# Kernel optimization log

Hardware: AMD Instinct MI355X
Metric: run time of the kernel (lower is better)

Reference implementation:

```python
import jax, jax.numpy as jnp
import numpy as np

D_MODEL = 1024
POOL = 2048
K = 16
D_FF = 4096
N_HEADS = 16
TEMP = 1.0
EPS = 1e-5


def _ln(x, g, b):
    mu = jnp.mean(x, axis=-1, keepdims=True)
    var = jnp.mean((x - mu) ** 2, axis=-1, keepdims=True)
    return (x - mu) * jax.lax.rsqrt(var + EPS) * g + b


def setup_inputs() -> dict:
    key = jax.random.key(0)
    ks = jax.random.split(key, 12)
    s = 0.02
    return {
        "x": jax.random.normal(ks[0], (4, 1024, D_MODEL), jnp.float32),
        "w_router": s * jax.random.normal(ks[1], (D_MODEL, POOL), jnp.float32),
        "b_router": jnp.zeros((POOL,), jnp.float32),
        "firing": s * jax.random.normal(ks[2], (POOL, D_FF), jnp.float32),
        "w_pool_out": s * jax.random.normal(ks[3], (D_FF, D_MODEL), jnp.float32),
        "b_pool_out": jnp.zeros((D_MODEL,), jnp.float32),
        "w_in": s * jax.random.normal(ks[4], (D_MODEL, 3 * D_MODEL), jnp.float32),
        "b_in": jnp.zeros((3 * D_MODEL,), jnp.float32),
        "w_attn_out": s * jax.random.normal(ks[5], (D_MODEL, D_MODEL), jnp.float32),
        "b_attn_out": jnp.zeros((D_MODEL,), jnp.float32),
        "g1": jnp.ones((D_MODEL,), jnp.float32),
        "beta1": jnp.zeros((D_MODEL,), jnp.float32),
        "g2": jnp.ones((D_MODEL,), jnp.float32),
        "beta2": jnp.zeros((D_MODEL,), jnp.float32),
    }


def reference(x, w_router, b_router, firing, w_pool_out, b_pool_out,
              w_in, b_in, w_attn_out, b_attn_out, g1, beta1, g2, beta2):
    B, S, D = x.shape
    Hd = D // N_HEADS
    # --- Context router: score every neuron, select top-k, softmax weights ---
    scores = x @ w_router + b_router                      # [B,S,P]
    top_vals, top_idx = jax.lax.top_k(scores, K)          # [B,S,K]
    weights = jax.nn.softmax(top_vals / TEMP, axis=-1)    # [B,S,K]
    # --- Neuron pool: gather firing patterns, weighted combine, GELU, project ---
    patterns = firing[top_idx]                            # [B,S,K,d_ff] gather
    combined = jnp.einsum('bsk,bskf->bsf', weights, patterns)  # [B,S,d_ff]
    neuron_out = jax.nn.gelu(combined, approximate=False) @ w_pool_out + b_pool_out  # [B,S,D]
    # --- Self-attention over neuron_out (dropout inactive at eval) ---
    qkv = neuron_out @ w_in + b_in                        # [B,S,3D]
    q, k, v = jnp.split(qkv, 3, axis=-1)
    q = q.reshape(B, S, N_HEADS, Hd).transpose(0, 2, 1, 3)
    k = k.reshape(B, S, N_HEADS, Hd).transpose(0, 2, 1, 3)
    v = v.reshape(B, S, N_HEADS, Hd).transpose(0, 2, 1, 3)
    logits = jnp.einsum('bhqd,bhkd->bhqk', q, k) / jnp.sqrt(jnp.float32(Hd))
    probs = jax.nn.softmax(logits, axis=-1)
    ctx = jnp.einsum('bhqk,bhkd->bhqd', probs, v)
    ctx = ctx.transpose(0, 2, 1, 3).reshape(B, S, D)
    attn_out = ctx @ w_attn_out + b_attn_out
    # --- Residuals + norms ---
    h = _ln(x + attn_out, g1, beta1)
    out = _ln(h + neuron_out, g2, beta2)
    return out
```

## Files before the change

kernel.cpp:

```cpp
#include <hip/hip_runtime.h>
#include <math.h>

typedef __attribute__((ext_vector_type(8))) __bf16 bf16x8;
typedef __attribute__((ext_vector_type(4))) __bf16 bf16x4;
typedef __attribute__((ext_vector_type(4))) float f32x4;

#define DEV static __device__ __forceinline__

DEV float b2f(unsigned short u){ union{unsigned i; float f;} c; c.i=((unsigned)u)<<16; return c.f; }
DEV unsigned short f2b(float f){
  union{float f; unsigned u;} c; c.f=f;
  unsigned r = 0x7FFFu + ((c.u>>16)&1u);
  return (unsigned short)((c.u + r)>>16);
}
DEV unsigned pack2(float a, float b){ return (unsigned)f2b(a) | ((unsigned)f2b(b)<<16); }
DEV float gelu_exact(float x){ return 0.5f*x*(1.f+erff(x*0.70710678118654752f)); }

typedef __attribute__((address_space(1))) void gas_void;
typedef __attribute__((address_space(3))) void las_void;
DEV void gload_lds16(const unsigned short* g, unsigned short* l){
  __builtin_amdgcn_global_load_lds((const gas_void*)g, (las_void*)l, 16, 0, 0);
}

template<int N> DEV void waitcnt_vm(){
  if constexpr(N==0)      asm volatile("s_waitcnt vmcnt(0)" ::: "memory");
  else if constexpr(N==2) asm volatile("s_waitcnt vmcnt(2)" ::: "memory");
  else if constexpr(N==3) asm volatile("s_waitcnt vmcnt(3)" ::: "memory");
  else if constexpr(N==4) asm volatile("s_waitcnt vmcnt(4)" ::: "memory");
  else if constexpr(N==6) asm volatile("s_waitcnt vmcnt(6)" ::: "memory");
  else if constexpr(N==8) asm volatile("s_waitcnt vmcnt(8)" ::: "memory");
  else                    asm volatile("s_waitcnt vmcnt(0)" ::: "memory");
}

__global__ __launch_bounds__(256) void k_cast_bf16(const float* __restrict__ in,
                                                   unsigned short* __restrict__ out, long n4)
{
  long i = (long)blockIdx.x*256 + threadIdx.x;
  if (i >= n4) return;
  float4 v = ((const float4*)in)[i];
  ushort4 o; o.x=f2b(v.x); o.y=f2b(v.y); o.z=f2b(v.z); o.w=f2b(v.w);
  ((ushort4*)out)[i] = o;
}

__global__ __launch_bounds__(256) void k_transpose_cast(const float* __restrict__ in,
                                                        unsigned short* __restrict__ out,
                                                        int R, int C)
{
  __shared__ float tile[32][33];
  const int tc = blockIdx.x*32, tr = blockIdx.y*32;
  {
    const int r = threadIdx.x>>3, c4 = (threadIdx.x&7)*4;
    float4 v = *(const float4*)&in[(long)(tr+r)*C + tc+c4];
    tile[r][c4+0]=v.x; tile[r][c4+1]=v.y; tile[r][c4+2]=v.z; tile[r][c4+3]=v.w;
  }
  __syncthreads();
  {
    const int c = threadIdx.x>>3, r4 = (threadIdx.x&7)*4;
    ushort4 o;
    o.x = f2b(tile[r4+0][c]); o.y = f2b(tile[r4+1][c]);
    o.z = f2b(tile[r4+2][c]); o.w = f2b(tile[r4+3][c]);
    *(ushort4*)&out[(long)(tc+c)*R + tr+r4] = o;
  }
}

template<int WR, int WC, int FM, int FN, int OMODE>
__global__ __launch_bounds__(WR*WC*64, 2) void k_gemm_bt(
  const unsigned short* __restrict__ A, long lda, long sAb,
  const unsigned short* __restrict__ Bt, long ldb, long sBb,
  float* __restrict__ Cf, unsigned short* __restrict__ Cb, long ldc, long sCb,
  const float* __restrict__ bias, int Kiters)
{
  constexpr int WAVES = WR*WC;
  constexpr int BM = WR*FM*16, BN = WC*FN*16;
  constexpr int AR16 = BM/16, TOT16 = (BM+BN)/16;
  constexpr int UNITS = TOT16/WAVES;
  static_assert(TOT16 % WAVES == 0, "stage units must split across waves");
  __shared__ __align__(16) unsigned short S[3][TOT16*512];
  const int tid = threadIdx.x;
  const int wave = tid>>6, lane = tid&63;
  const int wr = wave/WC, wc = wave%WC;
  const int l15 = lane&15, lhi = lane>>4;
  const int lrow = lane>>2;
  const int lcol = ((lane&3) ^ ((lrow>>1)&3))*8;

  const int gx = gridDim.x;
  const int nwg = gx*gridDim.y;
  const int id = blockIdx.y*gx + blockIdx.x;
  const int sid = (id&7)*(nwg>>3) + (id>>3);
  const long bm = (long)(sid / gx)*BM, bn = (long)(sid % gx)*BN;

  const unsigned short* Ab  = A  + (long)blockIdx.z*sAb + bm*lda;
  const unsigned short* Btb = Bt + (long)blockIdx.z*sBb + bn*ldb;

  f32x4 acc[FM][FN];
  #pragma unroll
  for (int i=0;i<FM;i++)
    #pragma unroll
    for (int j=0;j<FN;j++) acc[i][j] = (f32x4){0.f,0.f,0.f,0.f};

  auto STAGE = [&](int kt, int buf){
    const long k0 = (long)kt*32;
    #pragma unroll
    for (int u=0; u<UNITS; ++u) {
      const int t = wave + u*WAVES;
      const unsigned short* g;
      if (t < AR16) g = Ab  + (long)(t*16 + lrow)*lda + k0 + lcol;
      else          g = Btb + (long)((t-AR16)*16 + lrow)*ldb + k0 + lcol;
      gload_lds16(g, &S[buf][t*512]);
    }
  };
  auto COMPUTE = [&](int buf){
    const unsigned short* Sb = S[buf];
    bf16x8 bfr[FN];
    #pragma unroll
    for (int j=0;j<FN;j++) {
      const int r = wc*(FN*16) + j*16 + l15;
      bfr[j] = *(const bf16x8*)&Sb[BM*32 + r*32 + ((lhi ^ ((r>>1)&3))*8)];
    }
    #pragma unroll
    for (int i=0;i<FM;i++) {
      const int r = wr*(FM*16) + i*16 + l15;
      bf16x8 a = *(const bf16x8*)&Sb[r*32 + ((lhi ^ ((r>>1)&3))*8)];
      #pragma unroll
      for (int j=0;j<FN;j++)
        acc[i][j] = __builtin_amdgcn_mfma_f32_16x16x32_bf16(a, bfr[j], acc[i][j], 0,0,0);
    }
  };

  STAGE(0, 0);
  if (Kiters > 1) STAGE(1, 1);
  for (int kt=0; kt<Kiters; ++kt) {
    if (kt+1 < Kiters) waitcnt_vm<UNITS>();
    else               waitcnt_vm<0>();
    __builtin_amdgcn_s_barrier();
    __builtin_amdgcn_sched_barrier(0);
    COMPUTE(kt%3);
    if (kt+2 < Kiters) STAGE(kt+2, (kt+2)%3);
  }

  #pragma unroll
  for (int i=0;i<FM;i++) {
    #pragma unroll
    for (int j=0;j<FN;j++) {
      long col = bn + wc*(FN*16) + j*16 + l15;
      float bb = bias ? bias[col] : 0.f;
      #pragma unroll
      for (int q=0;q<4;q++) {
        long row = bm + wr*(FM*16) + i*16 + lhi*4 + q;
        float v = acc[i][j][q] + bb;
        long off = (long)blockIdx.z*sCb + row*ldc + col;
        if constexpr (OMODE==0 || OMODE==2) Cf[off] = v;
        if constexpr (OMODE==1 || OMODE==2) Cb[off] = f2b(v);
      }
    }
  }
}

__global__ __launch_bounds__(256) void k_combine_bias_bf16(
    const float* __restrict__ p, long sz, const float* __restrict__ bias,
    unsigned short* __restrict__ outb)
{
  const long t = blockIdx.x;
  const int tid = threadIdx.x;
  float4 a = ((const float4*)(p + t*1024))[tid];
  float4 b = ((const float4*)(p + sz + t*1024))[tid];
  float4 bi = ((const float4*)bias)[tid];
  ushort4 o;
  o.x = f2b(a.x+b.x+bi.x); o.y = f2b(a.y+b.y+bi.y);
  o.z = f2b(a.z+b.z+bi.z); o.w = f2b(a.w+b.w+bi.w);
  ((ushort4*)(outb + t*1024))[tid] = o;
}

__global__ __launch_bounds__(256) void k_topk_softmax(const float* __restrict__ scores,
                                                      int* __restrict__ topidx,
                                                      float* __restrict__ topw)
{
  const int tid = threadIdx.x, wave = tid>>6, lane = tid&63;
  const long t = blockIdx.x;
  const float* row = scores + t*2048;
  const int base = wave*512 + lane*8;
  unsigned k0,k1,k2,k3,k4,k5,k6,k7;
  {
    float4 a = *(const float4*)(row + base);
    float4 b = *(const float4*)(row + base + 4);
    float v[8] = {a.x,a.y,a.z,a.w,b.x,b.y,b.z,b.w};
    unsigned kk[8];
    #pragma unroll
    for (int e=0;e<8;e++){
      int bi = __float_as_int(v[e]);
      unsigned u = (bi<0) ? ~(unsigned)bi : ((unsigned)bi | 0x80000000u);
      kk[e] = (u & 0xFFFFF800u) | (unsigned)(2047 - (base+e));
    }
    k0=kk[0];k1=kk[1];k2=kk[2];k3=kk[3];k4=kk[4];k5=kk[5];k6=kk[6];k7=kk[7];
  }
  #define CX(x,y) { unsigned mx = x>y?x:y, mn = x>y?y:x; x=mx; y=mn; }
  CX(k0,k1) CX(k2,k3) CX(k4,k5) CX(k6,k7)
  CX(k0,k2) CX(k1,k3) CX(k4,k6) CX(k5,k7)
  CX(k1,k2) CX(k5,k6)
  CX(k0,k4) CX(k1,k5) CX(k2,k6) CX(k3,k7)
  CX(k2,k4) CX(k3,k5)
  CX(k1,k2) CX(k3,k4) CX(k5,k6)
  #undef CX

  __shared__ unsigned wk[4][16];
  unsigned my1 = 0;
  for (int it=0; it<16; ++it){
    unsigned best = k0;
    #pragma unroll
    for (int off=1; off<64; off<<=1){
      unsigned o = __shfl_xor(best, off);
      best = o>best ? o : best;
    }
    if (lane==it) my1 = best;
    bool own = (k0==best);
    k0 = own?k1:k0; k1 = own?k2:k1; k2 = own?k3:k2; k3 = own?k4:k3;
    k4 = own?k5:k4; k5 = own?k6:k5; k6 = own?k7:k6; k7 = own?0u:k7;
  }
  if (lane < 16) wk[wave][lane] = my1;
  __syncthreads();
  if (wave == 0){
    unsigned c = wk[lane>>4][lane&15];
    unsigned my2 = 0;
    for (int it=0; it<16; ++it){
      unsigned best = c;
      #pragma unroll
      for (int off=1; off<64; off<<=1){
        unsigned o = __shfl_xor(best, off);
        best = o>best ? o : best;
      }
      if (lane==it) my2 = best;
      c = (c==best) ? 0u : c;
    }
    int idx = 2047 - (int)(my2 & 0x7FFu);
    float val = -1e30f;
    if (lane < 16) val = row[idx];
    float m0 = __shfl(val, 0);
    float e = (lane < 16) ? __expf(val - m0) : 0.f;
    float s = e;
    #pragma unroll
    for (int off=1; off<64; off<<=1) s += __shfl_xor(s, off);
    if (lane < 16){
      topw[t*16+lane]   = e/s;
      topidx[t*16+lane] = idx;
    }
  }
}

__global__ __launch_bounds__(256) void k_gather_gelu(const int* __restrict__ topidx,
                                                     const float* __restrict__ topw,
                                                     const unsigned short* __restrict__ firing,
                                                     unsigned short* __restrict__ gact)
{
  __shared__ int idx[4][16]; __shared__ float w[4][16];
  const int tid = threadIdx.x;
  const int c = blockIdx.x & 7;
  const long t0 = (long)(blockIdx.x >> 3) * 4;
  if (tid < 64) {
    int tok = tid >> 4, k = tid & 15;
    idx[tok][k] = topidx[(t0+tok)*16 + k];
    w[tok][k]   = topw[(t0+tok)*16 + k];
  }
  __syncthreads();
  const int tok = tid >> 6, lane = tid & 63;
  const int f0 = c*512 + lane*8;
  float acc[8] = {0,0,0,0,0,0,0,0};
  #pragma unroll
  for (int k=0;k<16;k++) {
    uint4 v = *(const uint4*)(firing + (long)idx[tok][k]*4096 + f0);
    const unsigned short* pu = (const unsigned short*)&v;
    float wk = w[tok][k];
    #pragma unroll
    for (int e=0;e<8;e++) acc[e] += wk * b2f(pu[e]);
  }
  float g[8];
  #pragma unroll
  for (int e=0;e<8;e++) g[e] = gelu_exact(acc[e]);
  uint4 ov;
  ov.x = pack2(g[0],g[1]); ov.y = pack2(g[2],g[3]);
  ov.z = pack2(g[4],g[5]); ov.w = pack2(g[6],g[7]);
  *(uint4*)(gact + (t0+tok)*4096 + f0) = ov;
}

__global__ __launch_bounds__(256) void k_vtrans(const unsigned short* __restrict__ qkv,
                                                unsigned short* __restrict__ vT)
{
  __shared__ unsigned short tile[64][65];
  int bh = blockIdx.y; int b = bh>>4, h = bh&15;
  long t0 = (long)blockIdx.x*64;
  const int tid = threadIdx.x;
  #pragma unroll
  for (int s=0;s<16;s++) {
    int i = tid + s*256;
    int r = i>>6, c = i&63;
    tile[r][c] = qkv[ (long)(b*1024 + t0 + r)*3072 + 2048 + h*64 + c ];
  }
  __syncthreads();
  #pragma unroll
  for (int s=0;s<16;s++) {
    int i = tid + s*256;
    int c = i>>6, r = i&63;
    vT[ (long)bh*65536 + (long)c*1024 + t0 + r ] = tile[r][c];
  }
}

__global__ __launch_bounds__(512, 4) void k_flash_attn(
  const unsigned short* __restrict__ qkv,
  const unsigned short* __restrict__ vT,
  unsigned short* __restrict__ ctx)
{
  __shared__ __align__(16) unsigned short Ks[2][128*64];
  __shared__ __align__(16) unsigned short Vs[2][64*128];
  const int tid = threadIdx.x;
  const int wave = tid>>6, lane = tid&63;
  const int l15 = lane&15, lhi = lane>>4;
  const int bh = blockIdx.x, b = bh>>4, h = bh&15;
  const long q0 = (long)blockIdx.y*128;
  const unsigned short* Qg = qkv + ((long)b*1024 + q0)*3072 + h*64;
  const unsigned short* Kg = qkv + (long)b*1024*3072 + 1024 + h*64;
  const unsigned short* Vg = vT + (long)bh*65536;

  auto STAGE_KV = [&](int t, int s){
    const long kv0 = (long)t*128;
    const int sr = lane>>3, sc = (lane&7)^sr;
    #pragma unroll
    for (int uu=0; uu<2; ++uu){
      int u = wave + uu*8;
      gload_lds16(Kg + (kv0 + u*8 + sr)*3072 + sc*8, &Ks[s][u*512]);
    }
    const int vc = (lane&15) ^ ((wave&1)*4 + lhi);
    #pragma unroll
    for (int uu=0; uu<2; ++uu){
      int u = wave + uu*8;
      gload_lds16(Vg + (long)(u*4+lhi)*1024 + kv0 + vc*8, &Vs[s][u*512]);
    }
  };

  STAGE_KV(0, 0);

  bf16x8 qf[2];
  {
    const long r = wave*16 + l15;
    qf[0] = *(const bf16x8*)(Qg + r*3072 + lhi*8);
    qf[1] = *(const bf16x8*)(Qg + r*3072 + 32 + lhi*8);
  }
  __syncthreads();

  f32x4 acco[4];
  #pragma unroll
  for (int nf=0;nf<4;nf++) acco[nf] = (f32x4){0.f,0.f,0.f,0.f};
  float m_run = -1e30f, l_run = 0.f;

  int sel = 0;
  for (int t=0; t<8; ++t) {
    if (t < 7) STAGE_KV(t+1, sel^1);
    f32x4 accs[8];
    #pragma unroll
    for (int fk=0;fk<8;fk++){
      accs[fk] = (f32x4){0.f,0.f,0.f,0.f};
      const int r = fk*16 + l15;
      bf16x8 k0 = *(const bf16x8*)&Ks[sel][r*64 + ((lhi^(r&7))*8)];
      accs[fk] = __builtin_amdgcn_mfma_f32_16x16x32_bf16(k0, qf[0], accs[fk],0,0,0);
      bf16x8 k1 = *(const bf16x8*)&Ks[sel][r*64 + (((4+lhi)^(r&7))*8)];
      accs[fk] = __builtin_amdgcn_mfma_f32_16x16x32_bf16(k1, qf[1], accs[fk],0,0,0);
    }
    float mt = -1e30f;
    #pragma unroll
    for (int fk=0;fk<8;fk++)
      #pragma unroll
      for (int q=0;q<4;q++) mt = fmaxf(mt, accs[fk][q]);
    mt = fmaxf(mt, __shfl_xor(mt,16));
    mt = fmaxf(mt, __shfl_xor(mt,32));
    mt *= 0.125f;
    if (!__all(mt <= m_run + 8.f)) {
      float mnew = fmaxf(m_run, mt);
      float fj = __expf(m_run - mnew);
      l_run *= fj;
      #pragma unroll
      for (int q=0;q<4;q++){
        float fr = __shfl(fj, (lane&48)|(lhi*4+q));
        #pragma unroll
        for (int nf=0;nf<4;nf++) acco[nf][q] *= fr;
      }
      m_run = mnew;
    }
    bf16x8 pa[4];
    float ssum = 0.f;
    #pragma unroll
    for (int fk=0;fk<8;fk++)
      #pragma unroll
      for (int q=0;q<4;q++){
        float p = __expf(accs[fk][q]*0.125f - m_run);
        ssum += p;
        pa[fk>>1][(fk&1)*4+q] = (__bf16)p;
      }
    ssum += __shfl_xor(ssum,16);
    ssum += __shfl_xor(ssum,32);
    l_run += ssum;
    #pragma unroll
    for (int kk=0;kk<4;kk++)
      #pragma unroll
      for (int nf=0;nf<4;nf++){
        const int rv = nf*16 + l15;
        const int cb = kk*4 + (lhi>>1);
        bf16x4 v0 = *(const bf16x4*)&Vs[sel][rv*128 + (( cb   ^(l15&7))*8) + (lhi&1)*4];
        bf16x4 v1 = *(const bf16x4*)&Vs[sel][rv*128 + (((cb+2)^(l15&7))*8) + (lhi&1)*4];
        bf16x8 vb = __builtin_shufflevector(v0, v1, 0,1,2,3,4,5,6,7);
        acco[nf] = __builtin_amdgcn_mfma_f32_16x16x32_bf16(pa[kk], vb, acco[nf],0,0,0);
      }
    __syncthreads();
    sel ^= 1;
  }

  #pragma unroll
  for (int q=0;q<4;q++){
    float lr = __shfl(l_run, (lane&48)|(lhi*4+q));
    float inv = 1.f/lr;
    long row = q0 + wave*16 + lhi*4 + q;
    #pragma unroll
    for (int nf=0;nf<4;nf++)
      ctx[((long)b*1024 + row)*1024 + h*64 + nf*16 + l15] = f2b(acco[nf][q]*inv);
  }
}

__global__ __launch_bounds__(256) void k_ln_res_fb(const float* __restrict__ a,
                                                   const unsigned short* __restrict__ b,
                                                   const float* __restrict__ g,
                                                   const float* __restrict__ be,
                                                   float* __restrict__ out)
{
  const long t = blockIdx.x;
  const int tid = threadIdx.x;
  const int wave = tid>>6, lane = tid&63;
  float4 av = ((const float4*)(a + t*1024))[tid];
  ushort4 ub = ((const ushort4*)(b + t*1024))[tid];
  float4 sv = { av.x + b2f(ub.x), av.y + b2f(ub.y),
                av.z + b2f(ub.z), av.w + b2f(ub.w) };
  float sum = sv.x+sv.y+sv.z+sv.w;
  float sq  = sv.x*sv.x + sv.y*sv.y + sv.z*sv.z + sv.w*sv.w;
  #pragma unroll
  for (int off=32; off; off>>=1){ sum += __shfl_xor(sum,off); sq += __shfl_xor(sq,off); }
  __shared__ float s1[4], s2[4];
  if (lane==0){ s1[wave]=sum; s2[wave]=sq; }
  __syncthreads();
  sum = s1[0]+s1[1]+s1[2]+s1[3];
  sq  = s2[0]+s2[1]+s2[2]+s2[3];
  float mu  = sum * (1.f/1024.f);
  float var = sq * (1.f/1024.f) - mu*mu;
  float rs  = rsqrtf(var + 1e-5f);
  float4 gv  = ((const float4*)g)[tid];
  float4 bev = ((const float4*)be)[tid];
  float4 ov = { (sv.x-mu)*rs*gv.x + bev.x,
                (sv.y-mu)*rs*gv.y + bev.y,
                (sv.z-mu)*rs*gv.z + bev.z,
                (sv.w-mu)*rs*gv.w + bev.w };
  ((float4*)(out + t*1024))[tid] = ov;
}

extern "C" void kernel_launch(void* const* d_in, const int* in_sizes, int n_in,
                              void* d_out, int out_size, void* d_ws, size_t ws_size,
                              hipStream_t stream)
{
  const float* x        = (const float*)d_in[0];
  const float* w_router = (const float*)d_in[1];
  const float* b_router = (const float*)d_in[2];
  const float* firing   = (const float*)d_in[3];
  const float* w_pool   = (const float*)d_in[4];
  const float* b_pool   = (const float*)d_in[5];
  const float* w_in     = (const float*)d_in[6];
  const float* b_in     = (const float*)d_in[7];
  const float* w_ao     = (const float*)d_in[8];
  const float* b_ao     = (const float*)d_in[9];
  const float* g1       = (const float*)d_in[10];
  const float* be1      = (const float*)d_in[11];
  const float* g2       = (const float*)d_in[12];
  const float* be2      = (const float*)d_in[13];
  float* out = (float*)d_out;
  char* ws = (char*)d_ws;

  unsigned short* xb    = (unsigned short*)(ws + 0);
  unsigned short* wrT   = (unsigned short*)(ws + 8388608);
  unsigned short* firb  = (unsigned short*)(ws + 12582912);
  unsigned short* wpoT  = (unsigned short*)(ws + 29360128);
  unsigned short* winT  = (unsigned short*)(ws + 37748736);
  unsigned short* waoT  = (unsigned short*)(ws + 44040192);
  float*  scores        = (float*)(ws + 46137344);
  unsigned short* gact  = (unsigned short*)(ws + 46137344);
  int*    topi          = (int*)(ws + 79691776);
  float*  topw          = (float*)(ws + 79953920);
  unsigned short* attnb = (unsigned short*)(ws + 80216064);
  unsigned short* neub  = (unsigned short*)(ws + 96993280);
  unsigned short* qkvb  = (unsigned short*)(ws + 105381888);
  unsigned short* vT    = (unsigned short*)(ws + 130547712);
  unsigned short* ctx   = (unsigned short*)(ws + 138936320);
  float*  hbuf          = (float*)(ws + 147324928);
  float*  poolp         = (float*)(ws + 130547712);

  if (ws_size < 164102144u) return;

  k_cast_bf16<<<4096, 256, 0, stream>>>(x, xb, 4096L*1024/4);
  k_cast_bf16<<<8192, 256, 0, stream>>>(firing, firb, 2048L*4096/4);
  k_transpose_cast<<<dim3(2048/32, 1024/32), 256, 0, stream>>>(w_router, wrT, 1024, 2048);
  k_transpose_cast<<<dim3(1024/32, 4096/32), 256, 0, stream>>>(w_pool,   wpoT, 4096, 1024);
  k_transpose_cast<<<dim3(3072/32, 1024/32), 256, 0, stream>>>(w_in,     winT, 1024, 3072);
  k_transpose_cast<<<dim3(1024/32, 1024/32), 256, 0, stream>>>(w_ao,     waoT, 1024, 1024);

  k_gemm_bt<2,2,4,4,0><<<dim3(16,32,1),256,0,stream>>>(xb,1024,0, wrT,1024,0,
        scores,nullptr,2048,0, b_router, 32);
  k_topk_softmax<<<4096,256,0,stream>>>(scores, topi, topw);
  k_gather_gelu<<<8192,256,0,stream>>>(topi, topw, firb, gact);

  k_gemm_bt<2,2,4,4,0><<<dim3(8,32,2),256,0,stream>>>(gact,4096,2048, wpoT,4096,2048,
        poolp,nullptr,1024,4194304, nullptr, 64);
  k_combine_bias_bf16<<<4096,256,0,stream>>>(poolp, 4194304, b_pool, neub);

  k_gemm_bt<2,2,4,4,1><<<dim3(24,32,1),256,0,stream>>>(neub,1024,0, winT,1024,0,
        nullptr,qkvb,3072,0, b_in, 32);

  k_vtrans<<<dim3(16,64),256,0,stream>>>(qkvb, vT);
  k_flash_attn<<<dim3(64,8),512,0,stream>>>(qkvb, vT, ctx);

  k_gemm_bt<2,2,4,2,1><<<dim3(16,32,1),256,0,stream>>>(ctx,1024,0, waoT,1024,0,
        nullptr,attnb,1024,0, b_ao, 32);

  k_ln_res_fb<<<4096,256,0,stream>>>(x, attnb, g1, be1, hbuf);
  k_ln_res_fb<<<4096,256,0,stream>>>(hbuf, neub, g2, be2, out);
}
```

Baseline: 271.8 us.

## Store router scores and split-K partials in bf16, fuse the two layernorms

The router GEMM now writes scores as bf16 instead of fp32, and top-k reads bf16 keys, so 16-bit values with index tie-breaking are used for selection. The split-K partials of the pool projection are also stored in bf16, which halves the traffic into the combine kernel. The two residual layernorm kernels are merged into one, so the intermediate h buffer is never written or re-read. The cost is precision: bf16 scores can flip top-k choices when values nearly tie, and bf16 partial sums add rounding error.

```diff
diff --git a/kernel.cpp b/kernel.cpp
--- a/kernel.cpp
+++ b/kernel.cpp
@@ -157,39 +157,42 @@
 }
 
 __global__ __launch_bounds__(256) void k_combine_bias_bf16(
-    const float* __restrict__ p, long sz, const float* __restrict__ bias,
+    const unsigned short* __restrict__ p, long sz, const float* __restrict__ bias,
     unsigned short* __restrict__ outb)
 {
   const long t = blockIdx.x;
   const int tid = threadIdx.x;
-  float4 a = ((const float4*)(p + t*1024))[tid];
-  float4 b = ((const float4*)(p + sz + t*1024))[tid];
+  ushort4 a = ((const ushort4*)(p + t*1024))[tid];
+  ushort4 b = ((const ushort4*)(p + sz + t*1024))[tid];
   float4 bi = ((const float4*)bias)[tid];
   ushort4 o;
-  o.x = f2b(a.x+b.x+bi.x); o.y = f2b(a.y+b.y+bi.y);
-  o.z = f2b(a.z+b.z+bi.z); o.w = f2b(a.w+b.w+bi.w);
+  o.x = f2b(b2f(a.x)+b2f(b.x)+bi.x); o.y = f2b(b2f(a.y)+b2f(b.y)+bi.y);
+  o.z = f2b(b2f(a.z)+b2f(b.z)+bi.z); o.w = f2b(b2f(a.w)+b2f(b.w)+bi.w);
   ((ushort4*)(outb + t*1024))[tid] = o;
 }
 
-__global__ __launch_bounds__(256) void k_topk_softmax(const float* __restrict__ scores,
+__global__ __launch_bounds__(256) void k_topk_softmax(const unsigned short* __restrict__ scores,
                                                       int* __restrict__ topidx,
                                                       float* __restrict__ topw)
 {
   const int tid = threadIdx.x, wave = tid>>6, lane = tid&63;
   const long t = blockIdx.x;
-  const float* row = scores + t*2048;
+  const unsigned short* row = scores + t*2048;
   const int base = wave*512 + lane*8;
   unsigned k0,k1,k2,k3,k4,k5,k6,k7;
   {
-    float4 a = *(const float4*)(row + base);
-    float4 b = *(const float4*)(row + base + 4);
-    float v[8] = {a.x,a.y,a.z,a.w,b.x,b.y,b.z,b.w};
+    uint4 v4 = *(const uint4*)(row + base);
+    unsigned short u[8] = {
+      (unsigned short)(v4.x&0xFFFF),(unsigned short)(v4.x>>16),
+      (unsigned short)(v4.y&0xFFFF),(unsigned short)(v4.y>>16),
+      (unsigned short)(v4.z&0xFFFF),(unsigned short)(v4.z>>16),
+      (unsigned short)(v4.w&0xFFFF),(unsigned short)(v4.w>>16) };
     unsigned kk[8];
     #pragma unroll
     for (int e=0;e<8;e++){
-      int bi = __float_as_int(v[e]);
-      unsigned u = (bi<0) ? ~(unsigned)bi : ((unsigned)bi | 0x80000000u);
-      kk[e] = (u & 0xFFFFF800u) | (unsigned)(2047 - (base+e));
+      unsigned m = (u[e]&0x8000u) ? (unsigned)(~u[e] & 0xFFFFu)
+                                  : ((unsigned)u[e] | 0x8000u);
+      kk[e] = (m<<16) | (unsigned)(2047 - (base+e));
     }
     k0=kk[0];k1=kk[1];k2=kk[2];k3=kk[3];k4=kk[4];k5=kk[5];k6=kk[6];k7=kk[7];
   }
@@ -233,7 +236,7 @@
     }
     int idx = 2047 - (int)(my2 & 0x7FFu);
     float val = -1e30f;
-    if (lane < 16) val = row[idx];
+    if (lane < 16) val = b2f(row[idx]);
     float m0 = __shfl(val, 0);
     float e = (lane < 16) ? __expf(val - m0) : 0.f;
     float s = e;
@@ -422,24 +425,27 @@
   }
 }
 
-__global__ __launch_bounds__(256) void k_ln_res_fb(const float* __restrict__ a,
-                                                   const unsigned short* __restrict__ b,
-                                                   const float* __restrict__ g,
-                                                   const float* __restrict__ be,
-                                                   float* __restrict__ out)
+__global__ __launch_bounds__(256) void k_ln2(const float* __restrict__ x,
+                                             const unsigned short* __restrict__ attnb,
+                                             const unsigned short* __restrict__ neub,
+                                             const float* __restrict__ g1,
+                                             const float* __restrict__ be1,
+                                             const float* __restrict__ g2,
+                                             const float* __restrict__ be2,
+                                             float* __restrict__ out)
 {
   const long t = blockIdx.x;
   const int tid = threadIdx.x;
   const int wave = tid>>6, lane = tid&63;
-  float4 av = ((const float4*)(a + t*1024))[tid];
-  ushort4 ub = ((const ushort4*)(b + t*1024))[tid];
-  float4 sv = { av.x + b2f(ub.x), av.y + b2f(ub.y),
-                av.z + b2f(ub.z), av.w + b2f(ub.w) };
+  __shared__ float s1[4], s2[4], s3[4], s4[4];
+  float4 xv = ((const float4*)(x + t*1024))[tid];
+  ushort4 ua = ((const ushort4*)(attnb + t*1024))[tid];
+  float4 sv = { xv.x + b2f(ua.x), xv.y + b2f(ua.y),
+                xv.z + b2f(ua.z), xv.w + b2f(ua.w) };
   float sum = sv.x+sv.y+sv.z+sv.w;
   float sq  = sv.x*sv.x + sv.y*sv.y + sv.z*sv.z + sv.w*sv.w;
   #pragma unroll
   for (int off=32; off; off>>=1){ sum += __shfl_xor(sum,off); sq += __shfl_xor(sq,off); }
-  __shared__ float s1[4], s2[4];
   if (lane==0){ s1[wave]=sum; s2[wave]=sq; }
   __syncthreads();
   sum = s1[0]+s1[1]+s1[2]+s1[3];
@@ -447,12 +453,30 @@
   float mu  = sum * (1.f/1024.f);
   float var = sq * (1.f/1024.f) - mu*mu;
   float rs  = rsqrtf(var + 1e-5f);
-  float4 gv  = ((const float4*)g)[tid];
-  float4 bev = ((const float4*)be)[tid];
-  float4 ov = { (sv.x-mu)*rs*gv.x + bev.x,
-                (sv.y-mu)*rs*gv.y + bev.y,
-                (sv.z-mu)*rs*gv.z + bev.z,
-                (sv.w-mu)*rs*gv.w + bev.w };
+  float4 g1v  = ((const float4*)g1)[tid];
+  float4 be1v = ((const float4*)be1)[tid];
+  ushort4 un = ((const ushort4*)(neub + t*1024))[tid];
+  float4 hv = { (sv.x-mu)*rs*g1v.x + be1v.x + b2f(un.x),
+                (sv.y-mu)*rs*g1v.y + be1v.y + b2f(un.y),
+                (sv.z-mu)*rs*g1v.z + be1v.z + b2f(un.z),
+                (sv.w-mu)*rs*g1v.w + be1v.w + b2f(un.w) };
+  float sum2 = hv.x+hv.y+hv.z+hv.w;
+  float sq2  = hv.x*hv.x + hv.y*hv.y + hv.z*hv.z + hv.w*hv.w;
+  #pragma unroll
+  for (int off=32; off; off>>=1){ sum2 += __shfl_xor(sum2,off); sq2 += __shfl_xor(sq2,off); }
+  if (lane==0){ s3[wave]=sum2; s4[wave]=sq2; }
+  __syncthreads();
+  sum2 = s3[0]+s3[1]+s3[2]+s3[3];
+  sq2  = s4[0]+s4[1]+s4[2]+s4[3];
+  float mu2  = sum2 * (1.f/1024.f);
+  float var2 = sq2 * (1.f/1024.f) - mu2*mu2;
+  float rs2  = rsqrtf(var2 + 1e-5f);
+  float4 g2v  = ((const float4*)g2)[tid];
+  float4 be2v = ((const float4*)be2)[tid];
+  float4 ov = { (hv.x-mu2)*rs2*g2v.x + be2v.x,
+                (hv.y-mu2)*rs2*g2v.y + be2v.y,
+                (hv.z-mu2)*rs2*g2v.z + be2v.z,
+                (hv.w-mu2)*rs2*g2v.w + be2v.w };
   ((float4*)(out + t*1024))[tid] = ov;
 }
 
@@ -483,7 +507,7 @@
   unsigned short* wpoT  = (unsigned short*)(ws + 29360128);
   unsigned short* winT  = (unsigned short*)(ws + 37748736);
   unsigned short* waoT  = (unsigned short*)(ws + 44040192);
-  float*  scores        = (float*)(ws + 46137344);
+  unsigned short* scoresb = (unsigned short*)(ws + 46137344);
   unsigned short* gact  = (unsigned short*)(ws + 46137344);
   int*    topi          = (int*)(ws + 79691776);
   float*  topw          = (float*)(ws + 79953920);
@@ -492,8 +516,7 @@
   unsigned short* qkvb  = (unsigned short*)(ws + 105381888);
   unsigned short* vT    = (unsigned short*)(ws + 130547712);
   unsigned short* ctx   = (unsigned short*)(ws + 138936320);
-  float*  hbuf          = (float*)(ws + 147324928);
-  float*  poolp         = (float*)(ws + 130547712);
+  unsigned short* poolpb= (unsigned short*)(ws + 130547712);
 
   if (ws_size < 164102144u) return;
 
@@ -504,14 +527,14 @@
   k_transpose_cast<<<dim3(3072/32, 1024/32), 256, 0, stream>>>(w_in,     winT, 1024, 3072);
   k_transpose_cast<<<dim3(1024/32, 1024/32), 256, 0, stream>>>(w_ao,     waoT, 1024, 1024);
 
-  k_gemm_bt<2,2,4,4,0><<<dim3(16,32,1),256,0,stream>>>(xb,1024,0, wrT,1024,0,
-        scores,nullptr,2048,0, b_router, 32);
-  k_topk_softmax<<<4096,256,0,stream>>>(scores, topi, topw);
+  k_gemm_bt<2,2,4,4,1><<<dim3(16,32,1),256,0,stream>>>(xb,1024,0, wrT,1024,0,
+        nullptr,scoresb,2048,0, b_router, 32);
+  k_topk_softmax<<<4096,256,0,stream>>>(scoresb, topi, topw);
   k_gather_gelu<<<8192,256,0,stream>>>(topi, topw, firb, gact);
 
-  k_gemm_bt<2,2,4,4,0><<<dim3(8,32,2),256,0,stream>>>(gact,4096,2048, wpoT,4096,2048,
-        poolp,nullptr,1024,4194304, nullptr, 64);
-  k_combine_bias_bf16<<<4096,256,0,stream>>>(poolp, 4194304, b_pool, neub);
+  k_gemm_bt<2,2,4,4,1><<<dim3(8,32,2),256,0,stream>>>(gact,4096,2048, wpoT,4096,2048,
+        nullptr,poolpb,1024,4194304, nullptr, 64);
+  k_combine_bias_bf16<<<4096,256,0,stream>>>(poolpb, 4194304, b_pool, neub);
 
   k_gemm_bt<2,2,4,4,1><<<dim3(24,32,1),256,0,stream>>>(neub,1024,0, winT,1024,0,
         nullptr,qkvb,3072,0, b_in, 32);
@@ -522,6 +545,5 @@
   k_gemm_bt<2,2,4,2,1><<<dim3(16,32,1),256,0,stream>>>(ctx,1024,0, waoT,1024,0,
         nullptr,attnb,1024,0, b_ao, 32);
 
-  k_ln_res_fb<<<4096,256,0,stream>>>(x, attnb, g1, be1, hbuf);
-  k_ln_res_fb<<<4096,256,0,stream>>>(hbuf, neub, g2, be2, out);
-}
+  k_ln2<<<4096,256,0,stream>>>(x, attnb, neub, g1, be1, g2, be2, out);
+}
```

New measurement: 262.0 us. 1.04x faster.
